# Performance work log

Hardware: AMD Instinct MI355X
Metric: run time of the kernel (lower is better)

The kernel has to match this reference:

```python
import jax, jax.numpy as jnp
import numpy as np

B, T, K = 1024, 4096, 16
START, STOP = 14, 15  # tag_to_ix['<START>'], tag_to_ix['<STOP>']
NEG_INF = -10000.0


def setup_inputs() -> dict:
    key = jax.random.key(0)
    k1, k2, k3 = jax.random.split(key, 3)
    feats = jax.random.normal(k1, (B, T, K), dtype=jnp.float32)
    tags = jax.random.randint(k2, (B, T), 0, 14, dtype=jnp.int32)  # real tags only
    transitions = jax.random.normal(k3, (K, K), dtype=jnp.float32)
    # mimic __init__: never transition FROM anything to START... (row START) and never transition TO STOP as source
    transitions = transitions.at[START, :].set(NEG_INF).at[:, STOP].set(NEG_INF)
    return {"feats": feats, "tags": tags, "transitions": transitions}


def _crf_nll(feats, tags, transitions):
    # feats: [B, T, K] emissions; tags: [B, T]; transitions[j, i] = score(i -> j)
    b = feats.shape[0]

    # ---- forward algorithm (partition function), batched logsumexp scan ----
    alpha0 = jnp.full((b, K), NEG_INF, dtype=feats.dtype).at[:, START].set(0.0)

    def step(alpha, feat_t):
        # alpha: [B, K] (prev tag i), feat_t: [B, K] (next tag j)
        # next_tag_var[b, j, i] = alpha[b, i] + trans[j, i] + feat_t[b, j]
        new = jax.nn.logsumexp(alpha[:, None, :] + transitions[None, :, :], axis=-1) + feat_t
        return new, None

    alpha, _ = jax.lax.scan(step, alpha0, jnp.swapaxes(feats, 0, 1))  # scan over T
    forward_score = jax.nn.logsumexp(alpha + transitions[STOP][None, :], axis=-1)  # [B]

    # ---- gold sentence score ----
    start_col = jnp.full((b, 1), START, dtype=tags.dtype)
    tags_ext = jnp.concatenate([start_col, tags], axis=1)  # [B, T+1]
    trans_score = transitions[tags_ext[:, 1:], tags_ext[:, :-1]].sum(axis=1)  # [B]
    emit_score = jnp.take_along_axis(feats, tags[:, :, None].astype(jnp.int32), axis=2)[..., 0].sum(axis=1)  # [B]
    gold_score = trans_score + emit_score + transitions[STOP, tags[:, -1]]  # [B]

    return forward_score - gold_score  # per-sequence NLL, [B]


def reference(feats, tags, transitions):
    return _crf_nll(feats, tags, transitions)
```

## Files before the change

### kernel.cpp

```cpp
#include <hip/hip_runtime.h>
#include <math.h>

#define B_TOT 1024
#define T_LEN 4096
#define K_TAGS 16
#define START_TAG 14
#define STOP_TAG 15

#define LOG2E 1.4426950408889634f
#define LN2 0.6931471805599453f

#define CH 64
#define NCH (T_LEN / CH)
#define NCHH (NCH / 2)
#define ROWW 1032
#define FBW (4 * ROWW)
#define FBTOT 9728

#define WS_VF 0
#define WS_VB 16384
#define WS_GF 32768
#define WS_GB 33792
#define WS_CF 34816
#define WS_CB 35840

typedef __attribute__((address_space(1))) const void GVoid;
typedef __attribute__((address_space(3))) void LVoid;

#define MATVEC_FWD(SV, EFV, EFNV, FNV, NEGCV, ET)                                     \
  do {                                                                                \
    float a0_, a1_, a2_, a3_, efa_, efn_;                                             \
    asm("v_mul_f32 %[a0], %[s], %[e0]\n\t"                                            \
        "v_fma_f32 %[efa], %[fn], %[l2e], %[nc]\n\t"                                  \
        "v_mul_f32_dpp %[a1], %[s], %[e1] row_ror:1 row_mask:0xf bank_mask:0xf\n\t"   \
        "v_mul_f32_dpp %[a2], %[s], %[e2] row_ror:2 row_mask:0xf bank_mask:0xf\n\t"   \
        "v_mul_f32_dpp %[a3], %[s], %[e3] row_ror:3 row_mask:0xf bank_mask:0xf\n\t"   \
        "v_fmac_f32_dpp %[a0], %[s], %[e4] row_ror:4 row_mask:0xf bank_mask:0xf\n\t"  \
        "v_fmac_f32_dpp %[a1], %[s], %[e5] row_ror:5 row_mask:0xf bank_mask:0xf\n\t"  \
        "v_fmac_f32_dpp %[a2], %[s], %[e6] row_ror:6 row_mask:0xf bank_mask:0xf\n\t"  \
        "v_fmac_f32_dpp %[a3], %[s], %[e7] row_ror:7 row_mask:0xf bank_mask:0xf\n\t"  \
        "v_fmac_f32_dpp %[a0], %[s], %[e8] row_ror:8 row_mask:0xf bank_mask:0xf\n\t"  \
        "v_fmac_f32_dpp %[a1], %[s], %[e9] row_ror:9 row_mask:0xf bank_mask:0xf\n\t"  \
        "v_fmac_f32_dpp %[a2], %[s], %[e10] row_ror:10 row_mask:0xf bank_mask:0xf\n\t"\
        "v_fmac_f32_dpp %[a3], %[s], %[e11] row_ror:11 row_mask:0xf bank_mask:0xf\n\t"\
        "v_fmac_f32_dpp %[a0], %[s], %[e12] row_ror:12 row_mask:0xf bank_mask:0xf\n\t"\
        "v_fmac_f32_dpp %[a1], %[s], %[e13] row_ror:13 row_mask:0xf bank_mask:0xf\n\t"\
        "v_fmac_f32_dpp %[a2], %[s], %[e14] row_ror:14 row_mask:0xf bank_mask:0xf\n\t"\
        "v_fmac_f32_dpp %[a3], %[s], %[e15] row_ror:15 row_mask:0xf bank_mask:0xf\n\t"\
        "v_exp_f32 %[efn], %[efa]\n\t"                                                \
        "v_add_f32 %[a0], %[a0], %[a1]\n\t"                                           \
        "v_add_f32 %[a2], %[a2], %[a3]\n\t"                                           \
        "v_add_f32 %[a0], %[a0], %[a2]\n\t"                                           \
        "v_mul_f32 %[s], %[a0], %[ef]"                                                \
        : [s] "+v"(SV), [a0] "=&v"(a0_), [a1] "=&v"(a1_), [a2] "=&v"(a2_),            \
          [a3] "=&v"(a3_), [efa] "=&v"(efa_), [efn] "=&v"(efn_)                       \
        : [ef] "v"(EFV), [fn] "v"(FNV), [l2e] "v"(LOG2E), [nc] "v"(NEGCV),            \
          [e0] "v"(ET[0]), [e1] "v"(ET[1]), [e2] "v"(ET[2]), [e3] "v"(ET[3]),         \
          [e4] "v"(ET[4]), [e5] "v"(ET[5]), [e6] "v"(ET[6]), [e7] "v"(ET[7]),         \
          [e8] "v"(ET[8]), [e9] "v"(ET[9]), [e10] "v"(ET[10]), [e11] "v"(ET[11]),     \
          [e12] "v"(ET[12]), [e13] "v"(ET[13]), [e14] "v"(ET[14]), [e15] "v"(ET[15]));\
    EFNV = efn_;                                                                      \
  } while (0)

#define MATVEC_BWD(SV, EFV, EFNV, FNV, NEGCV, ET)                                     \
  do {                                                                                \
    float a0_, a1_, a2_, a3_, efa_, efn_, us_;                                        \
    asm("v_mul_f32 %[us], %[s], %[ef]\n\t"                                            \
        "v_fma_f32 %[efa], %[fn], %[l2e], %[nc]\n\t"                                  \
        "v_mul_f32 %[a0], %[us], %[e0]\n\t"                                           \
        "v_mul_f32_dpp %[a1], %[us], %[e1] row_ror:1 row_mask:0xf bank_mask:0xf\n\t"  \
        "v_mul_f32_dpp %[a2], %[us], %[e2] row_ror:2 row_mask:0xf bank_mask:0xf\n\t"  \
        "v_mul_f32_dpp %[a3], %[us], %[e3] row_ror:3 row_mask:0xf bank_mask:0xf\n\t"  \
        "v_fmac_f32_dpp %[a0], %[us], %[e4] row_ror:4 row_mask:0xf bank_mask:0xf\n\t" \
        "v_fmac_f32_dpp %[a1], %[us], %[e5] row_ror:5 row_mask:0xf bank_mask:0xf\n\t" \
        "v_fmac_f32_dpp %[a2], %[us], %[e6] row_ror:6 row_mask:0xf bank_mask:0xf\n\t" \
        "v_fmac_f32_dpp %[a3], %[us], %[e7] row_ror:7 row_mask:0xf bank_mask:0xf\n\t" \
        "v_fmac_f32_dpp %[a0], %[us], %[e8] row_ror:8 row_mask:0xf bank_mask:0xf\n\t" \
        "v_fmac_f32_dpp %[a1], %[us], %[e9] row_ror:9 row_mask:0xf bank_mask:0xf\n\t" \
        "v_fmac_f32_dpp %[a2], %[us], %[e10] row_ror:10 row_mask:0xf bank_mask:0xf\n\t"\
        "v_fmac_f32_dpp %[a3], %[us], %[e11] row_ror:11 row_mask:0xf bank_mask:0xf\n\t"\
        "v_fmac_f32_dpp %[a0], %[us], %[e12] row_ror:12 row_mask:0xf bank_mask:0xf\n\t"\
        "v_fmac_f32_dpp %[a1], %[us], %[e13] row_ror:13 row_mask:0xf bank_mask:0xf\n\t"\
        "v_fmac_f32_dpp %[a2], %[us], %[e14] row_ror:14 row_mask:0xf bank_mask:0xf\n\t"\
        "v_fmac_f32_dpp %[a3], %[us], %[e15] row_ror:15 row_mask:0xf bank_mask:0xf\n\t"\
        "v_exp_f32 %[efn], %[efa]\n\t"                                                \
        "v_add_f32 %[a0], %[a0], %[a1]\n\t"                                           \
        "v_add_f32 %[a2], %[a2], %[a3]\n\t"                                           \
        "v_add_f32 %[s], %[a0], %[a2]"                                                \
        : [s] "+v"(SV), [us] "=&v"(us_), [a0] "=&v"(a0_), [a1] "=&v"(a1_),            \
          [a2] "=&v"(a2_), [a3] "=&v"(a3_), [efa] "=&v"(efa_), [efn] "=&v"(efn_)      \
        : [ef] "v"(EFV), [fn] "v"(FNV), [l2e] "v"(LOG2E), [nc] "v"(NEGCV),            \
          [e0] "v"(ET[0]), [e1] "v"(ET[1]), [e2] "v"(ET[2]), [e3] "v"(ET[3]),         \
          [e4] "v"(ET[4]), [e5] "v"(ET[5]), [e6] "v"(ET[6]), [e7] "v"(ET[7]),         \
          [e8] "v"(ET[8]), [e9] "v"(ET[9]), [e10] "v"(ET[10]), [e11] "v"(ET[11]),     \
          [e12] "v"(ET[12]), [e13] "v"(ET[13]), [e14] "v"(ET[14]), [e15] "v"(ET[15]));\
    EFNV = efn_;                                                                      \
  } while (0)

__global__ __launch_bounds__(128, 1) void crf_half_kernel(
        const float* __restrict__ feats,
        const int* __restrict__ tags,
        const float* __restrict__ trans,
        float* __restrict__ ws) {
    __shared__ float FBraw[2][FBTOT];
    __shared__ int TG[2][2][4 * CH];
    __shared__ float TlS[K_TAGS * K_TAGS];
    __shared__ int edgeRow[2][4];

    const int tid = threadIdx.x;
    const int wid = tid >> 6;
    const int lane = tid & 63;
    const int r = lane >> 4;
    const int j = lane & 15;
    const int half = wid;
    const int bbase = blockIdx.x * 4;

    float* const FB = &FBraw[wid][128];

    for (int i = tid; i < K_TAGS * K_TAGS; i += 128) TlS[i] = trans[i];
    if (lane < 4) edgeRow[wid][lane] = half ? STOP_TAG : START_TAG;
    __syncthreads();

    const int pv = __builtin_amdgcn_mov_dpp(j, 0x121, 0xF, 0xF, false);
    const int d = (pv - j) & 15;

    float et[K_TAGS];
#pragma unroll
    for (int i = 0; i < K_TAGS; ++i) {
        const int src = (j + d * i) & 15;
        et[i] = exp2f(TlS[half ? (src * K_TAGS + j) : (j * K_TAGS + src)] * LOG2E);
    }

    const int rowbase = (lane & ~15) << 2;

    auto stage = [&](int c, int pb) {
        const int t0 = c * CH;
#pragma unroll
        for (int i = 0; i < 16; ++i) {
            const int row = i >> 2, seg = i & 3;
            const float* g = feats + ((size_t)(bbase + row) * T_LEN + t0) * K_TAGS
                             + seg * 256 + lane * 4;
            const float* l = &FB[pb * FBW + row * ROWW + seg * 256];
            __builtin_amdgcn_global_load_lds((GVoid*)g, (LVoid*)l, 16, 0, 0);
        }
#pragma unroll
        for (int row = 0; row < 4; ++row) {
            const int* g = tags + (size_t)(bbase + row) * T_LEN + t0 + lane;
            const int* l = &TG[wid][pb][row * CH];
            __builtin_amdgcn_global_load_lds((GVoid*)g, (LVoid*)l, 4, 0, 0);
        }
    };

    float s = half ? exp2f(TlS[STOP_TAG * K_TAGS + j] * LOG2E)
                   : ((j == START_TAG) ? 1.0f : 0.0f);
    int Cacc = 0;
    float bp = 1.0f;
    float ef = 1.0f;
    float gold = 0.0f;

    if (!half) {
        stage(0, 0);
        for (int c = 0; c < NCHH; ++c) {
            const int pb = c & 1;
            if (c + 1 < NCHH) {
                stage(c + 1, pb ^ 1);
                __builtin_amdgcn_s_waitcnt(0x4F74);
            } else {
                __builtin_amdgcn_s_waitcnt(0x0F70);
            }
            __builtin_amdgcn_sched_barrier(0);

            const float* fp = &FB[pb * FBW + r * ROWW + j];
            float fr[8];
#pragma unroll
            for (int u = 0; u < 8; ++u) fr[u] = fp[u * 16];
            ef = exp2f(fmaf(fr[0], LOG2E, -4.0f));

            for (int tb = 0; tb < CH; tb += 8) {
                const float* fq = fp + (tb + 8) * 16;
#pragma unroll
                for (int u = 0; u < 8; ++u) {
                    const float fn = fr[(u + 1) & 7];
                    fr[u] = fq[u * 16];

                    float negc;
                    if (u == 6) {
                        const int kprev = (((__float_as_int(bp) >> 23) & 0xFF) - 127);
                        Cacc += 32 + kprev;
                        negc = -(4.0f + (float)kprev);
                    } else {
                        negc = -4.0f;
                    }

                    float efn;
                    MATVEC_FWD(s, ef, efn, fn, negc, et);
                    ef = efn;

                    if (u == 7)
                        bp = __int_as_float(__builtin_amdgcn_ds_bpermute(
                                rowbase, __float_as_int(s)));
                }
            }

            {
                const int* tg = &TG[wid][pb][r * CH];
                const int t4 = j * 4;
                const int pidx = (j == 0) ? 0 : (t4 - 1);
                const int pval = tg[pidx];
                int prev = (j == 0) ? edgeRow[wid][r] : pval;
                const float* fbase = &FB[pb * FBW + r * ROWW];
#pragma unroll
                for (int q = 0; q < 4; ++q) {
                    const int tc = tg[t4 + q];
                    gold += TlS[tc * K_TAGS + prev];
                    gold += fbase[(t4 + q) * 16 + tc];
                    prev = tc;
                }
                if (j == 15) edgeRow[wid][r] = prev;
            }
        }
    } else {
        stage(NCH - 1, 0);
        for (int ii = 0; ii < NCHH; ++ii) {
            const int pb = ii & 1;
            if (ii + 1 < NCHH) {
                stage(NCH - 2 - ii, pb ^ 1);
                __builtin_amdgcn_s_waitcnt(0x4F74);
            } else {
                __builtin_amdgcn_s_waitcnt(0x0F70);
            }
            __builtin_amdgcn_sched_barrier(0);

            const float* fp = &FB[pb * FBW + r * ROWW + j];
            float fr[8];
#pragma unroll
            for (int u = 0; u < 8; ++u) fr[u] = fp[(CH - 1 - u) * 16];
            ef = exp2f(fmaf(fr[0], LOG2E, -4.0f));

            for (int tb = 0; tb < CH; tb += 8) {
                const float* fq = fp + (CH - 9 - tb) * 16;
#pragma unroll
                for (int u = 0; u < 8; ++u) {
                    const float fn = fr[(u + 1) & 7];
                    fr[u] = fq[-(u * 16)];

                    float negc;
                    if (u == 6) {
                        const int kprev = (((__float_as_int(bp) >> 23) & 0xFF) - 127);
                        Cacc += 32 + kprev;
                        negc = -(4.0f + (float)kprev);
                    } else {
                        negc = -4.0f;
                    }

                    float efn;
                    MATVEC_BWD(s, ef, efn, fn, negc, et);
                    ef = efn;

                    if (u == 7)
                        bp = __int_as_float(__builtin_amdgcn_ds_bpermute(
                                rowbase, __float_as_int(s)));
                }
            }

            {
                const int* tg = &TG[wid][pb][r * CH];
                const int t4 = j * 4;
                const float* fbase = &FB[pb * FBW + r * ROWW];
                const int nlast = (j == 15) ? edgeRow[wid][r] : tg[t4 + 4];
#pragma unroll
                for (int q = 0; q < 4; ++q) {
                    const int tc = tg[t4 + q];
                    const int tn = (q == 3) ? nlast : tg[t4 + q + 1];
                    gold += TlS[tn * K_TAGS + tc];
                    gold += fbase[(t4 + q) * 16 + tc];
                }
                if (j == 0) edgeRow[wid][r] = tg[0];
            }
        }
    }

    float gg = gold;
#pragma unroll
    for (int dd = 1; dd < 16; dd <<= 1) gg += __shfl_xor(gg, dd, 16);

    const int b = bbase + r;
    if (!half) {
        ws[WS_VF + b * 16 + j] = s;
        if (j == 0) {
            ((int*)ws)[WS_CF + b] = Cacc;
            const int tn = tags[(size_t)b * T_LEN + (T_LEN / 2)];
            ws[WS_GF + b] = gg + TlS[tn * K_TAGS + edgeRow[wid][r]];
        }
    } else {
        ws[WS_VB + b * 16 + j] = s;
        if (j == 0) {
            ((int*)ws)[WS_CB + b] = Cacc;
            ws[WS_GB + b] = gg;
        }
    }
}

__global__ __launch_bounds__(64) void crf_combine(
        const float* __restrict__ ws, float* __restrict__ out) {
    const int b = blockIdx.x * 64 + threadIdx.x;
    const float* vf = ws + WS_VF + b * 16;
    const float* vb = ws + WS_VB + b * 16;
    float dot = 0.0f;
#pragma unroll
    for (int t = 0; t < 16; ++t) dot = fmaf(vf[t], vb[t], dot);
    const int cf = ((const int*)ws)[WS_CF + b];
    const int cb = ((const int*)ws)[WS_CB + b];
    const float g = ws[WS_GF + b] + ws[WS_GB + b];
    out[b] = LN2 * (log2f(dot) + (float)(cf + cb)) - g;
}

extern "C" void kernel_launch(void* const* d_in, const int* in_sizes, int n_in,
                              void* d_out, int out_size, void* d_ws, size_t ws_size,
                              hipStream_t stream) {
    const float* feats = (const float*)d_in[0];
    const int* tags = (const int*)d_in[1];
    const float* trans = (const float*)d_in[2];
    float* out = (float*)d_out;
    float* ws = (float*)d_ws;

    crf_half_kernel<<<dim3(B_TOT / 4), dim3(128), 0, stream>>>(feats, tags, trans, ws);
    crf_combine<<<dim3(B_TOT / 64), dim3(64), 0, stream>>>(ws, out);
}
```

Before: 437.0 us.

## Split each 16-wide matvec across two lane groups joined by permlane32 swap

Each wave now handles 2 sequences instead of 4. Each sequence's 16-term transition matvec is split into two 8-term halves held in different 16-lane rows, and the partial sums are combined with a permlane32_swap followed by a DPP row rotate. The block grows to 256 threads (4 waves) for the same 4 sequences per block. The aim is to halve the serial dependent FMA chain per time step and give more waves to hide latency. In exchange it adds a cross-lane swap and a DPP move to the critical path, duplicates the gold-score work across the redundant lanes, and doubles LDS staging per sequence.

```diff
diff --git a/kernel.cpp b/kernel.cpp
--- a/kernel.cpp
+++ b/kernel.cpp
@@ -14,8 +14,8 @@
 #define NCH (T_LEN / CH)
 #define NCHH (NCH / 2)
 #define ROWW 1032
-#define FBW (4 * ROWW)
-#define FBTOT 9728
+#define FBW2 (2 * ROWW)
+#define FBTOT 5120
 
 #define WS_VF 0
 #define WS_VB 16384
@@ -26,133 +26,120 @@
 
 typedef __attribute__((address_space(1))) const void GVoid;
 typedef __attribute__((address_space(3))) void LVoid;
-
-#define MATVEC_FWD(SV, EFV, EFNV, FNV, NEGCV, ET)                                     \
-  do {                                                                                \
-    float a0_, a1_, a2_, a3_, efa_, efn_;                                             \
-    asm("v_mul_f32 %[a0], %[s], %[e0]\n\t"                                            \
-        "v_fma_f32 %[efa], %[fn], %[l2e], %[nc]\n\t"                                  \
-        "v_mul_f32_dpp %[a1], %[s], %[e1] row_ror:1 row_mask:0xf bank_mask:0xf\n\t"   \
-        "v_mul_f32_dpp %[a2], %[s], %[e2] row_ror:2 row_mask:0xf bank_mask:0xf\n\t"   \
-        "v_mul_f32_dpp %[a3], %[s], %[e3] row_ror:3 row_mask:0xf bank_mask:0xf\n\t"   \
-        "v_fmac_f32_dpp %[a0], %[s], %[e4] row_ror:4 row_mask:0xf bank_mask:0xf\n\t"  \
-        "v_fmac_f32_dpp %[a1], %[s], %[e5] row_ror:5 row_mask:0xf bank_mask:0xf\n\t"  \
-        "v_fmac_f32_dpp %[a2], %[s], %[e6] row_ror:6 row_mask:0xf bank_mask:0xf\n\t"  \
-        "v_fmac_f32_dpp %[a3], %[s], %[e7] row_ror:7 row_mask:0xf bank_mask:0xf\n\t"  \
-        "v_fmac_f32_dpp %[a0], %[s], %[e8] row_ror:8 row_mask:0xf bank_mask:0xf\n\t"  \
-        "v_fmac_f32_dpp %[a1], %[s], %[e9] row_ror:9 row_mask:0xf bank_mask:0xf\n\t"  \
-        "v_fmac_f32_dpp %[a2], %[s], %[e10] row_ror:10 row_mask:0xf bank_mask:0xf\n\t"\
-        "v_fmac_f32_dpp %[a3], %[s], %[e11] row_ror:11 row_mask:0xf bank_mask:0xf\n\t"\
-        "v_fmac_f32_dpp %[a0], %[s], %[e12] row_ror:12 row_mask:0xf bank_mask:0xf\n\t"\
-        "v_fmac_f32_dpp %[a1], %[s], %[e13] row_ror:13 row_mask:0xf bank_mask:0xf\n\t"\
-        "v_fmac_f32_dpp %[a2], %[s], %[e14] row_ror:14 row_mask:0xf bank_mask:0xf\n\t"\
-        "v_fmac_f32_dpp %[a3], %[s], %[e15] row_ror:15 row_mask:0xf bank_mask:0xf\n\t"\
-        "v_exp_f32 %[efn], %[efa]\n\t"                                                \
-        "v_add_f32 %[a0], %[a0], %[a1]\n\t"                                           \
-        "v_add_f32 %[a2], %[a2], %[a3]\n\t"                                           \
-        "v_add_f32 %[a0], %[a0], %[a2]\n\t"                                           \
-        "v_mul_f32 %[s], %[a0], %[ef]"                                                \
-        : [s] "+v"(SV), [a0] "=&v"(a0_), [a1] "=&v"(a1_), [a2] "=&v"(a2_),            \
-          [a3] "=&v"(a3_), [efa] "=&v"(efa_), [efn] "=&v"(efn_)                       \
-        : [ef] "v"(EFV), [fn] "v"(FNV), [l2e] "v"(LOG2E), [nc] "v"(NEGCV),            \
-          [e0] "v"(ET[0]), [e1] "v"(ET[1]), [e2] "v"(ET[2]), [e3] "v"(ET[3]),         \
-          [e4] "v"(ET[4]), [e5] "v"(ET[5]), [e6] "v"(ET[6]), [e7] "v"(ET[7]),         \
-          [e8] "v"(ET[8]), [e9] "v"(ET[9]), [e10] "v"(ET[10]), [e11] "v"(ET[11]),     \
-          [e12] "v"(ET[12]), [e13] "v"(ET[13]), [e14] "v"(ET[14]), [e15] "v"(ET[15]));\
-    EFNV = efn_;                                                                      \
+typedef unsigned u32x2 __attribute__((ext_vector_type(2)));
+
+#define MATVEC8_FWD(SV, PARTV, EFAV, FNV, NEGCV, ET)                                  \
+  do {                                                                               \
+    float a0_, a1_, a2_, a3_;                                                        \
+    asm("v_mul_f32 %[a0], %[s], %[e0]\n\t"                                           \
+        "v_fma_f32 %[efa], %[fn], %[l2e], %[nc]\n\t"                                 \
+        "v_mul_f32_dpp %[a1], %[s], %[e1] row_ror:1 row_mask:0xf bank_mask:0xf\n\t"  \
+        "v_mul_f32_dpp %[a2], %[s], %[e2] row_ror:2 row_mask:0xf bank_mask:0xf\n\t"  \
+        "v_mul_f32_dpp %[a3], %[s], %[e3] row_ror:3 row_mask:0xf bank_mask:0xf\n\t"  \
+        "v_fmac_f32_dpp %[a0], %[s], %[e4] row_ror:4 row_mask:0xf bank_mask:0xf\n\t" \
+        "v_fmac_f32_dpp %[a1], %[s], %[e5] row_ror:5 row_mask:0xf bank_mask:0xf\n\t" \
+        "v_fmac_f32_dpp %[a2], %[s], %[e6] row_ror:6 row_mask:0xf bank_mask:0xf\n\t" \
+        "v_fmac_f32_dpp %[a3], %[s], %[e7] row_ror:7 row_mask:0xf bank_mask:0xf\n\t" \
+        "v_add_f32 %[a0], %[a0], %[a1]\n\t"                                          \
+        "v_add_f32 %[a2], %[a2], %[a3]\n\t"                                          \
+        "v_add_f32 %[part], %[a0], %[a2]"                                            \
+        : [part] "=&v"(PARTV), [efa] "=&v"(EFAV), [a0] "=&v"(a0_),                   \
+          [a1] "=&v"(a1_), [a2] "=&v"(a2_), [a3] "=&v"(a3_)                          \
+        : [s] "v"(SV), [fn] "v"(FNV), [l2e] "v"(LOG2E), [nc] "v"(NEGCV),             \
+          [e0] "v"(ET[0]), [e1] "v"(ET[1]), [e2] "v"(ET[2]), [e3] "v"(ET[3]),        \
+          [e4] "v"(ET[4]), [e5] "v"(ET[5]), [e6] "v"(ET[6]), [e7] "v"(ET[7]));       \
   } while (0)
 
-#define MATVEC_BWD(SV, EFV, EFNV, FNV, NEGCV, ET)                                     \
-  do {                                                                                \
-    float a0_, a1_, a2_, a3_, efa_, efn_, us_;                                        \
-    asm("v_mul_f32 %[us], %[s], %[ef]\n\t"                                            \
-        "v_fma_f32 %[efa], %[fn], %[l2e], %[nc]\n\t"                                  \
-        "v_mul_f32 %[a0], %[us], %[e0]\n\t"                                           \
-        "v_mul_f32_dpp %[a1], %[us], %[e1] row_ror:1 row_mask:0xf bank_mask:0xf\n\t"  \
-        "v_mul_f32_dpp %[a2], %[us], %[e2] row_ror:2 row_mask:0xf bank_mask:0xf\n\t"  \
-        "v_mul_f32_dpp %[a3], %[us], %[e3] row_ror:3 row_mask:0xf bank_mask:0xf\n\t"  \
-        "v_fmac_f32_dpp %[a0], %[us], %[e4] row_ror:4 row_mask:0xf bank_mask:0xf\n\t" \
-        "v_fmac_f32_dpp %[a1], %[us], %[e5] row_ror:5 row_mask:0xf bank_mask:0xf\n\t" \
-        "v_fmac_f32_dpp %[a2], %[us], %[e6] row_ror:6 row_mask:0xf bank_mask:0xf\n\t" \
-        "v_fmac_f32_dpp %[a3], %[us], %[e7] row_ror:7 row_mask:0xf bank_mask:0xf\n\t" \
-        "v_fmac_f32_dpp %[a0], %[us], %[e8] row_ror:8 row_mask:0xf bank_mask:0xf\n\t" \
-        "v_fmac_f32_dpp %[a1], %[us], %[e9] row_ror:9 row_mask:0xf bank_mask:0xf\n\t" \
-        "v_fmac_f32_dpp %[a2], %[us], %[e10] row_ror:10 row_mask:0xf bank_mask:0xf\n\t"\
-        "v_fmac_f32_dpp %[a3], %[us], %[e11] row_ror:11 row_mask:0xf bank_mask:0xf\n\t"\
-        "v_fmac_f32_dpp %[a0], %[us], %[e12] row_ror:12 row_mask:0xf bank_mask:0xf\n\t"\
-        "v_fmac_f32_dpp %[a1], %[us], %[e13] row_ror:13 row_mask:0xf bank_mask:0xf\n\t"\
-        "v_fmac_f32_dpp %[a2], %[us], %[e14] row_ror:14 row_mask:0xf bank_mask:0xf\n\t"\
-        "v_fmac_f32_dpp %[a3], %[us], %[e15] row_ror:15 row_mask:0xf bank_mask:0xf\n\t"\
-        "v_exp_f32 %[efn], %[efa]\n\t"                                                \
-        "v_add_f32 %[a0], %[a0], %[a1]\n\t"                                           \
-        "v_add_f32 %[a2], %[a2], %[a3]\n\t"                                           \
-        "v_add_f32 %[s], %[a0], %[a2]"                                                \
-        : [s] "+v"(SV), [us] "=&v"(us_), [a0] "=&v"(a0_), [a1] "=&v"(a1_),            \
-          [a2] "=&v"(a2_), [a3] "=&v"(a3_), [efa] "=&v"(efa_), [efn] "=&v"(efn_)      \
-        : [ef] "v"(EFV), [fn] "v"(FNV), [l2e] "v"(LOG2E), [nc] "v"(NEGCV),            \
-          [e0] "v"(ET[0]), [e1] "v"(ET[1]), [e2] "v"(ET[2]), [e3] "v"(ET[3]),         \
-          [e4] "v"(ET[4]), [e5] "v"(ET[5]), [e6] "v"(ET[6]), [e7] "v"(ET[7]),         \
-          [e8] "v"(ET[8]), [e9] "v"(ET[9]), [e10] "v"(ET[10]), [e11] "v"(ET[11]),     \
-          [e12] "v"(ET[12]), [e13] "v"(ET[13]), [e14] "v"(ET[14]), [e15] "v"(ET[15]));\
-    EFNV = efn_;                                                                      \
+#define MATVEC8_BWD(SV, EFV, PARTV, EFAV, FNV, NEGCV, ET)                            \
+  do {                                                                               \
+    float a0_, a1_, a2_, a3_, us_;                                                   \
+    asm("v_mul_f32 %[us], %[s], %[ef]\n\t"                                           \
+        "v_fma_f32 %[efa], %[fn], %[l2e], %[nc]\n\t"                                 \
+        "v_mul_f32 %[a0], %[us], %[e0]\n\t"                                          \
+        "v_mul_f32_dpp %[a1], %[us], %[e1] row_ror:1 row_mask:0xf bank_mask:0xf\n\t" \
+        "v_mul_f32_dpp %[a2], %[us], %[e2] row_ror:2 row_mask:0xf bank_mask:0xf\n\t" \
+        "v_mul_f32_dpp %[a3], %[us], %[e3] row_ror:3 row_mask:0xf bank_mask:0xf\n\t" \
+        "v_fmac_f32_dpp %[a0], %[us], %[e4] row_ror:4 row_mask:0xf bank_mask:0xf\n\t"\
+        "v_fmac_f32_dpp %[a1], %[us], %[e5] row_ror:5 row_mask:0xf bank_mask:0xf\n\t"\
+        "v_fmac_f32_dpp %[a2], %[us], %[e6] row_ror:6 row_mask:0xf bank_mask:0xf\n\t"\
+        "v_fmac_f32_dpp %[a3], %[us], %[e7] row_ror:7 row_mask:0xf bank_mask:0xf\n\t"\
+        "v_add_f32 %[a0], %[a0], %[a1]\n\t"                                          \
+        "v_add_f32 %[a2], %[a2], %[a3]\n\t"                                          \
+        "v_add_f32 %[part], %[a0], %[a2]"                                            \
+        : [part] "=&v"(PARTV), [efa] "=&v"(EFAV), [us] "=&v"(us_),                   \
+          [a0] "=&v"(a0_), [a1] "=&v"(a1_), [a2] "=&v"(a2_), [a3] "=&v"(a3_)         \
+        : [s] "v"(SV), [ef] "v"(EFV), [fn] "v"(FNV), [l2e] "v"(LOG2E),               \
+          [nc] "v"(NEGCV),                                                           \
+          [e0] "v"(ET[0]), [e1] "v"(ET[1]), [e2] "v"(ET[2]), [e3] "v"(ET[3]),        \
+          [e4] "v"(ET[4]), [e5] "v"(ET[5]), [e6] "v"(ET[6]), [e7] "v"(ET[7]));       \
   } while (0)
 
-__global__ __launch_bounds__(128, 1) void crf_half_kernel(
+__device__ __forceinline__ float xadd32(float x) {
+    u32x2 t = __builtin_amdgcn_permlane32_swap(__float_as_uint(x), __float_as_uint(x),
+                                               false, false);
+    return __uint_as_float(t.x) + __uint_as_float(t.y);
+}
+
+__global__ __launch_bounds__(256, 1) void crf_half_kernel(
         const float* __restrict__ feats,
         const int* __restrict__ tags,
         const float* __restrict__ trans,
         float* __restrict__ ws) {
-    __shared__ float FBraw[2][FBTOT];
-    __shared__ int TG[2][2][4 * CH];
+    __shared__ float FBraw[4][FBTOT];
+    __shared__ int TG[4][2][2 * CH];
     __shared__ float TlS[K_TAGS * K_TAGS];
-    __shared__ int edgeRow[2][4];
+    __shared__ int edgeRow[4][2];
 
     const int tid = threadIdx.x;
     const int wid = tid >> 6;
     const int lane = tid & 63;
     const int r = lane >> 4;
     const int j = lane & 15;
-    const int half = wid;
-    const int bbase = blockIdx.x * 4;
+    const int half = wid & 1;
+    const int bpair = blockIdx.x * 4 + (wid >> 1) * 2;
+    const int rb = r & 1;
+    const int cp = r >> 1;
+    const int b = bpair + rb;
 
     float* const FB = &FBraw[wid][128];
 
-    for (int i = tid; i < K_TAGS * K_TAGS; i += 128) TlS[i] = trans[i];
-    if (lane < 4) edgeRow[wid][lane] = half ? STOP_TAG : START_TAG;
+    for (int i = tid; i < K_TAGS * K_TAGS; i += 256) TlS[i] = trans[i];
+    if (lane < 2) edgeRow[wid][lane] = half ? STOP_TAG : START_TAG;
     __syncthreads();
 
     const int pv = __builtin_amdgcn_mov_dpp(j, 0x121, 0xF, 0xF, false);
     const int d = (pv - j) & 15;
 
-    float et[K_TAGS];
-#pragma unroll
-    for (int i = 0; i < K_TAGS; ++i) {
-        const int src = (j + d * i) & 15;
+    float et[8];
+#pragma unroll
+    for (int i = 0; i < 8; ++i) {
+        const int src = (j + d * i + cp * 8) & 15;
         et[i] = exp2f(TlS[half ? (src * K_TAGS + j) : (j * K_TAGS + src)] * LOG2E);
     }
 
-    const int rowbase = (lane & ~15) << 2;
+    const int colj = (j + cp * 8) & 15;
+    const int rowbase = rb << 6;
 
     auto stage = [&](int c, int pb) {
         const int t0 = c * CH;
 #pragma unroll
-        for (int i = 0; i < 16; ++i) {
+        for (int i = 0; i < 8; ++i) {
             const int row = i >> 2, seg = i & 3;
-            const float* g = feats + ((size_t)(bbase + row) * T_LEN + t0) * K_TAGS
+            const float* g = feats + ((size_t)(bpair + row) * T_LEN + t0) * K_TAGS
                              + seg * 256 + lane * 4;
-            const float* l = &FB[pb * FBW + row * ROWW + seg * 256];
+            const float* l = &FB[pb * FBW2 + row * ROWW + seg * 256];
             __builtin_amdgcn_global_load_lds((GVoid*)g, (LVoid*)l, 16, 0, 0);
         }
 #pragma unroll
-        for (int row = 0; row < 4; ++row) {
-            const int* g = tags + (size_t)(bbase + row) * T_LEN + t0 + lane;
+        for (int row = 0; row < 2; ++row) {
+            const int* g = tags + (size_t)(bpair + row) * T_LEN + t0 + lane;
             const int* l = &TG[wid][pb][row * CH];
             __builtin_amdgcn_global_load_lds((GVoid*)g, (LVoid*)l, 4, 0, 0);
         }
     };
 
-    float s = half ? exp2f(TlS[STOP_TAG * K_TAGS + j] * LOG2E)
-                   : ((j == START_TAG) ? 1.0f : 0.0f);
+    float s = half ? exp2f(TlS[STOP_TAG * K_TAGS + colj] * LOG2E)
+                   : ((colj == START_TAG) ? 1.0f : 0.0f);
     int Cacc = 0;
     float bp = 1.0f;
     float ef = 1.0f;
@@ -164,13 +151,13 @@
             const int pb = c & 1;
             if (c + 1 < NCHH) {
                 stage(c + 1, pb ^ 1);
-                __builtin_amdgcn_s_waitcnt(0x4F74);
+                __builtin_amdgcn_s_waitcnt(0x0F7A);
             } else {
                 __builtin_amdgcn_s_waitcnt(0x0F70);
             }
             __builtin_amdgcn_sched_barrier(0);
 
-            const float* fp = &FB[pb * FBW + r * ROWW + j];
+            const float* fp = &FB[pb * FBW2 + rb * ROWW + colj];
             float fr[8];
 #pragma unroll
             for (int u = 0; u < 8; ++u) fr[u] = fp[u * 16];
@@ -192,8 +179,17 @@
                         negc = -4.0f;
                     }
 
-                    float efn;
-                    MATVEC_FWD(s, ef, efn, fn, negc, et);
+                    float part, efa;
+                    MATVEC8_FWD(s, part, efa, fn, negc, et);
+                    const float sum = xadd32(part);
+
+                    float snew, efn;
+                    asm("v_mul_f32 %[sv], %[sum], %[ef]\n\t"
+                        "v_exp_f32 %[efn], %[efa]\n\t"
+                        "v_mul_f32_dpp %[sv], %[sum], %[ef] row_ror:8 row_mask:0xc bank_mask:0xf"
+                        : [sv] "=&v"(snew), [efn] "=&v"(efn)
+                        : [sum] "v"(sum), [ef] "v"(ef), [efa] "v"(efa));
+                    s = snew;
                     ef = efn;
 
                     if (u == 7)
@@ -203,12 +199,12 @@
             }
 
             {
-                const int* tg = &TG[wid][pb][r * CH];
+                const int* tg = &TG[wid][pb][rb * CH];
                 const int t4 = j * 4;
                 const int pidx = (j == 0) ? 0 : (t4 - 1);
                 const int pval = tg[pidx];
-                int prev = (j == 0) ? edgeRow[wid][r] : pval;
-                const float* fbase = &FB[pb * FBW + r * ROWW];
+                int prev = (j == 0) ? edgeRow[wid][rb] : pval;
+                const float* fbase = &FB[pb * FBW2 + rb * ROWW];
 #pragma unroll
                 for (int q = 0; q < 4; ++q) {
                     const int tc = tg[t4 + q];
@@ -216,7 +212,7 @@
                     gold += fbase[(t4 + q) * 16 + tc];
                     prev = tc;
                 }
-                if (j == 15) edgeRow[wid][r] = prev;
+                if (j == 15 && r < 2) edgeRow[wid][rb] = prev;
             }
         }
     } else {
@@ -225,13 +221,13 @@
             const int pb = ii & 1;
             if (ii + 1 < NCHH) {
                 stage(NCH - 2 - ii, pb ^ 1);
-                __builtin_amdgcn_s_waitcnt(0x4F74);
+                __builtin_amdgcn_s_waitcnt(0x0F7A);
             } else {
                 __builtin_amdgcn_s_waitcnt(0x0F70);
             }
             __builtin_amdgcn_sched_barrier(0);
 
-            const float* fp = &FB[pb * FBW + r * ROWW + j];
+            const float* fp = &FB[pb * FBW2 + rb * ROWW + colj];
             float fr[8];
 #pragma unroll
             for (int u = 0; u < 8; ++u) fr[u] = fp[(CH - 1 - u) * 16];
@@ -253,8 +249,17 @@
                         negc = -4.0f;
                     }
 
-                    float efn;
-                    MATVEC_BWD(s, ef, efn, fn, negc, et);
+                    float part, efa;
+                    MATVEC8_BWD(s, ef, part, efa, fn, negc, et);
+                    const float sum = xadd32(part);
+
+                    float snew, efn;
+                    asm("v_mov_b32 %[sv], %[sum]\n\t"
+                        "v_exp_f32 %[efn], %[efa]\n\t"
+                        "v_mov_b32_dpp %[sv], %[sum] row_ror:8 row_mask:0xc bank_mask:0xf"
+                        : [sv] "=&v"(snew), [efn] "=&v"(efn)
+                        : [sum] "v"(sum), [efa] "v"(efa));
+                    s = snew;
                     ef = efn;
 
                     if (u == 7)
@@ -264,10 +269,10 @@
             }
 
             {
-                const int* tg = &TG[wid][pb][r * CH];
+                const int* tg = &TG[wid][pb][rb * CH];
                 const int t4 = j * 4;
-                const float* fbase = &FB[pb * FBW + r * ROWW];
-                const int nlast = (j == 15) ? edgeRow[wid][r] : tg[t4 + 4];
+                const float* fbase = &FB[pb * FBW2 + rb * ROWW];
+                const int nlast = (j == 15) ? edgeRow[wid][rb] : tg[t4 + 4];
 #pragma unroll
                 for (int q = 0; q < 4; ++q) {
                     const int tc = tg[t4 + q];
@@ -275,7 +280,7 @@
                     gold += TlS[tn * K_TAGS + tc];
                     gold += fbase[(t4 + q) * 16 + tc];
                 }
-                if (j == 0) edgeRow[wid][r] = tg[0];
+                if (j == 0 && r < 2) edgeRow[wid][rb] = tg[0];
             }
         }
     }
@@ -284,19 +289,20 @@
 #pragma unroll
     for (int dd = 1; dd < 16; dd <<= 1) gg += __shfl_xor(gg, dd, 16);
 
-    const int b = bbase + r;
-    if (!half) {
-        ws[WS_VF + b * 16 + j] = s;
-        if (j == 0) {
-            ((int*)ws)[WS_CF + b] = Cacc;
-            const int tn = tags[(size_t)b * T_LEN + (T_LEN / 2)];
-            ws[WS_GF + b] = gg + TlS[tn * K_TAGS + edgeRow[wid][r]];
-        }
-    } else {
-        ws[WS_VB + b * 16 + j] = s;
-        if (j == 0) {
-            ((int*)ws)[WS_CB + b] = Cacc;
-            ws[WS_GB + b] = gg;
+    if (r < 2) {
+        if (!half) {
+            ws[WS_VF + b * 16 + j] = s;
+            if (j == 0) {
+                ((int*)ws)[WS_CF + b] = Cacc;
+                const int tn = tags[(size_t)b * T_LEN + (T_LEN / 2)];
+                ws[WS_GF + b] = gg + TlS[tn * K_TAGS + edgeRow[wid][rb]];
+            }
+        } else {
+            ws[WS_VB + b * 16 + j] = s;
+            if (j == 0) {
+                ((int*)ws)[WS_CB + b] = Cacc;
+                ws[WS_GB + b] = gg;
+            }
         }
     }
 }
@@ -324,6 +330,6 @@
     float* out = (float*)d_out;
     float* ws = (float*)d_ws;
 
-    crf_half_kernel<<<dim3(B_TOT / 4), dim3(128), 0, stream>>>(feats, tags, trans, ws);
+    crf_half_kernel<<<dim3(B_TOT / 4), dim3(256), 0, stream>>>(feats, tags, trans, ws);
     crf_combine<<<dim3(B_TOT / 64), dim3(64), 0, stream>>>(ws, out);
 }
```

After: 417.3 us. 4.5% less time.
